# Kernel optimization log

Measured on AMD Instinct MI355X. Metric: run time of the kernel, lower is better.

## Reference

```python
import jax, jax.numpy as jnp
import numpy as np

ALPHA = 0.2        # LeakyReLU negative slope (config['alpha'])
NEG_INF = -9e15    # mask value from the original code


def setup_inputs() -> dict:
    key = jax.random.key(0)
    k1, k2, k3, k4 = jax.random.split(key, 4)
    N, Fin, Fout = 8192, 512, 256
    inp = jax.random.normal(k1, (N, Fin), dtype=jnp.float32)
    adj = jax.random.randint(k2, (N, N), 0, 2, dtype=jnp.int32)
    # xavier_uniform with gain=1.414
    limW = 1.414 * np.sqrt(6.0 / (Fin + Fout))
    W = jax.random.uniform(k3, (Fin, Fout), dtype=jnp.float32, minval=-limW, maxval=limW)
    lima = 1.414 * np.sqrt(6.0 / (2 * Fout + 1))
    a = jax.random.uniform(k4, (2 * Fout, 1), dtype=jnp.float32, minval=-lima, maxval=lima)
    return {"input": inp, "adj": adj, "W": W, "a": a}


def reference(input, adj, W, a):
    # h: [N, F]
    h = input @ W
    Fout = W.shape[1]
    # The original builds a_input[i, j] = concat(h_i, h_j) and dots with a.
    # Equivalently: e_ij = leakyrelu(h_i . a[:F] + h_j . a[F:]), computed
    # without the O(N^2 * 2F) intermediate.
    s1 = h @ a[:Fout, 0]   # [N] contribution from node i
    s2 = h @ a[Fout:, 0]   # [N] contribution from node j
    e = s1[:, None] + s2[None, :]                     # [N, N]
    e = jnp.where(e > 0, e, ALPHA * e)                # LeakyReLU
    scores = jnp.where(adj > 0, e, NEG_INF)
    attention = jax.nn.softmax(scores, axis=1)        # row-wise softmax
    # dropout is identity in inference mode (training=False)
    h_prime = attention @ h                           # [N, F]
    return jax.nn.elu(h_prime)                        # concat=True path
```

## Files before the change

### kernel.cpp

```cpp
#include <hip/hip_runtime.h>
#include <stdint.h>
#include <stddef.h>


#define N_NODES 8192
#define FIN     512
#define FOUT    256
#define LRALPHA 0.2f
#define MI_SHIFT 16.0f

typedef float f32x4 __attribute__((ext_vector_type(4)));
typedef short s16x8 __attribute__((ext_vector_type(8)));
typedef unsigned short u16x4 __attribute__((ext_vector_type(4)));
typedef int   i32x4 __attribute__((ext_vector_type(4)));
typedef unsigned long long u64;

__device__ __forceinline__ short f2bf_rne(float f) {
  uint32_t u = __builtin_bit_cast(uint32_t, f);
  u += 0x7fffu + ((u >> 16) & 1u);
  return (short)(u >> 16);
}
__device__ __forceinline__ short f2bf_fast(float f) {
  uint32_t u = __builtin_bit_cast(uint32_t, f);
  return (short)((u + 0x8000u) >> 16);
}
__device__ __forceinline__ float bf2f(short s) {
  uint32_t u = ((uint32_t)(uint16_t)s) << 16;
  return __builtin_bit_cast(float, u);
}

__global__ __launch_bounds__(256) void k_prep(const float* __restrict__ W,
                                              uint16_t* __restrict__ WThi,
                                              uint16_t* __restrict__ WTlo) {
  const int idx = blockIdx.x * 256 + threadIdx.x;
  const int n = idx >> 9;
  const int k = idx & 511;
  float v = W[k * FOUT + n];
  short h = f2bf_rne(v);
  WThi[idx] = (uint16_t)h;
  WTlo[idx] = (uint16_t)f2bf_rne(v - bf2f(h));
}

__global__ __launch_bounds__(256, 4) void k_pre(const float* __restrict__ X,
                                                const uint16_t* __restrict__ WThi,
                                                const uint16_t* __restrict__ WTlo,
                                                const float* __restrict__ a,
                                                const int* __restrict__ adj,
                                                uint16_t* __restrict__ HTf,
                                                float* __restrict__ s1g,
                                                float* __restrict__ s2g,
                                                u64* __restrict__ M3) {
  __shared__ float ls1[16], ls2[16];
  __shared__ uint16_t tile[FOUT * 16];
  const int lane = threadIdx.x & 63;
  const int w    = threadIdx.x >> 6;

  if (blockIdx.x >= 512) {
    const int bxm  = blockIdx.x - 512;
    const int iblk = bxm >> 5;
    const int jc   = bxm & 31;
    const int L    = lane;
    const int* base = adj + (size_t)(iblk * 128 + w * 32) * N_NODES + jc * 256 + L;
    u64 keep0 = 0, keep1 = 0, keep2 = 0, keep3 = 0;
#pragma unroll
    for (int it = 0; it < 32; ++it) {
      const int* rp = base + (size_t)it * N_NODES;
      int v0 = rp[0], v1 = rp[64], v2 = rp[128], v3 = rp[192];
      u64 b0 = __ballot(v0 != 0);
      u64 b1 = __ballot(v1 != 0);
      u64 b2 = __ballot(v2 != 0);
      u64 b3 = __ballot(v3 != 0);
      if (L == it) { keep0 = b0; keep1 = b1; keep2 = b2; keep3 = b3; }
    }
    if (L < 32) {
      const size_t mb = (size_t)iblk * 128 * 128 + (w * 32 + L);
      M3[mb + (size_t)(jc * 4 + 0) * 128] = keep0;
      M3[mb + (size_t)(jc * 4 + 1) * 128] = keep1;
      M3[mb + (size_t)(jc * 4 + 2) * 128] = keep2;
      M3[mb + (size_t)(jc * 4 + 3) * 128] = keep3;
    }
    return;
  }

  const int m    = lane & 15;
  const int quad = lane >> 4;
  const int i0   = blockIdx.x * 16;
  const int colg = w * 64;

  f32x4 acc[4];
#pragma unroll
  for (int cb = 0; cb < 4; ++cb) { f32x4 z = {0.f,0.f,0.f,0.f}; acc[cb] = z; }

  for (int kt = 0; kt < FIN / 32; ++kt) {
    const int k0 = kt * 32 + quad * 8;
    const float* ap = X + (size_t)(i0 + m) * FIN + k0;
    f32x4 a0 = *(const f32x4*)ap;
    f32x4 a1 = *(const f32x4*)(ap + 4);
    s16x8 ahi, alo;
#pragma unroll
    for (int e = 0; e < 4; ++e) {
      short h0 = f2bf_rne(a0[e]); ahi[e] = h0; alo[e] = f2bf_rne(a0[e] - bf2f(h0));
      short h1 = f2bf_rne(a1[e]); ahi[4+e] = h1; alo[4+e] = f2bf_rne(a1[e] - bf2f(h1));
    }
#pragma unroll
    for (int cb = 0; cb < 4; ++cb) {
      const int n = colg + cb * 16 + m;
      s16x8 bhi = *(const s16x8*)(WThi + (size_t)n * FIN + k0);
      s16x8 blo = *(const s16x8*)(WTlo + (size_t)n * FIN + k0);
      acc[cb] = __builtin_amdgcn_mfma_f32_16x16x32_bf16(ahi, bhi, acc[cb], 0, 0, 0);
      acc[cb] = __builtin_amdgcn_mfma_f32_16x16x32_bf16(ahi, blo, acc[cb], 0, 0, 0);
      acc[cb] = __builtin_amdgcn_mfma_f32_16x16x32_bf16(alo, bhi, acc[cb], 0, 0, 0);
    }
  }

  float p1[4] = {0.f,0.f,0.f,0.f}, p2[4] = {0.f,0.f,0.f,0.f};
#pragma unroll
  for (int cb = 0; cb < 4; ++cb) {
    const int n = colg + cb * 16 + m;
    const float a1c = a[n];
    const float a2c = a[FOUT + n];
#pragma unroll
    for (int reg = 0; reg < 4; ++reg) {
      p1[reg] += acc[cb][reg] * a1c;
      p2[reg] += acc[cb][reg] * a2c;
    }
  }
#pragma unroll
  for (int off = 1; off <= 8; off <<= 1)
#pragma unroll
    for (int reg = 0; reg < 4; ++reg) {
      p1[reg] += __shfl_xor(p1[reg], off);
      p2[reg] += __shfl_xor(p2[reg], off);
    }
  if (threadIdx.x < 16) { ls1[threadIdx.x] = 0.f; ls2[threadIdx.x] = 0.f; }
  __syncthreads();
  if (m == 0) {
#pragma unroll
    for (int reg = 0; reg < 4; ++reg) {
      atomicAdd(&ls1[quad * 4 + reg], p1[reg]);
      atomicAdd(&ls2[quad * 4 + reg], p2[reg]);
    }
  }
#pragma unroll
  for (int cb = 0; cb < 4; ++cb) {
    const int col = colg + cb * 16 + m;
    u16x4 pk;
#pragma unroll
    for (int reg = 0; reg < 4; ++reg) pk[reg] = (uint16_t)f2bf_rne(acc[cb][reg]);
    *(u16x4*)(tile + col * 16 + quad * 4) = pk;
  }
  __syncthreads();
  const int t = threadIdx.x;
  if (t < 16) { s1g[i0 + t] = ls1[t]; s2g[i0 + t] = ls2[t]; }
  const int jt = i0 >> 5;
  const int qh = (i0 >> 4) & 1;
  const int c  = t >> 4;
  const int mm = t & 15;
#pragma unroll
  for (int qq = 0; qq < 2; ++qq) {
    uint4 v = *(const uint4*)(tile + (c * 16 + mm) * 16 + qq * 8);
    *(uint4*)(HTf + ((((size_t)jt * 16 + c) * 64) + (qh * 2 + qq) * 16 + mm) * 8) = v;
  }
}

__global__ __launch_bounds__(512, 4) void k_attn(const u64* __restrict__ M3,
                                                 const uint16_t* __restrict__ HTf,
                                                 const float* __restrict__ s1,
                                                 const float* __restrict__ s2,
                                                 float* __restrict__ pout,
                                                 float* __restrict__ pden,
                                                 int split) {
  __shared__ uint16_t PL[2][4096];
  __shared__ float lss2[1024];
  __shared__ float ldsden[512];

  const int tid  = threadIdx.x;
  const int lane = tid & 63;
  const int w    = tid >> 6;
  const int m    = lane & 15;
  const int q    = lane >> 4;
  const int rg   = w >> 2, cg = w & 3;
  const int r    = tid & 127;
  const int cpr  = tid >> 7;
  const int i0   = blockIdx.x * 128;
  const int sp   = blockIdx.y;
  const int jrange = N_NODES / split;
  const int jbeg   = sp * jrange;
  const int nphase = jrange / 32;

  const float s1r = s1[i0 + r];
  float mi = fmaxf(s1r + MI_SHIFT, LRALPHA * (s1r + MI_SHIFT));

  f32x4 acc[4][4];
#pragma unroll
  for (int rt = 0; rt < 4; ++rt)
#pragma unroll
    for (int cb = 0; cb < 4; ++cb) { f32x4 z = {0.f,0.f,0.f,0.f}; acc[rt][cb] = z; }
  float den = 0.f;

  const u64* mrow = M3 + ((size_t)blockIdx.x * 128 + (jbeg >> 6)) * 128 + r;
  u64 mcur = mrow[0];

#pragma unroll 1
  for (int ph = 0; ph < nphase; ph += 2) {
    if ((ph & 31) == 0) {
      __syncthreads();
      if (tid < 256) *(f32x4*)(lss2 + tid * 4) =
        *(const f32x4*)(s2 + jbeg + (ph >> 5) * 1024 + tid * 4);
      __syncthreads();
    }
    u64 mnx = (ph + 2 < nphase) ? mrow[((ph >> 1) + 1) * 128] : 0;
#pragma unroll
    for (int po = 0; po < 2; ++po) {
      const int p = ph + po;
      const int pl = p & 31;
      f32x4 sA = *(const f32x4*)(lss2 + pl * 32 + cpr * 8);
      f32x4 sB = *(const f32x4*)(lss2 + pl * 32 + cpr * 8 + 4);
      const uint32_t by = (uint32_t)(mcur >> ((po * 4 + cpr) * 8)) & 0xffu;
      s16x8 P0;
#pragma unroll
      for (int e = 0; e < 4; ++e) {
        float x0 = s1r + sA[e];
        float pv0 = __expf(fmaxf(x0, LRALPHA * x0) - mi);
        pv0 = ((by >> e) & 1u) ? pv0 : 0.f;
        den += pv0; P0[e] = f2bf_fast(pv0);
        float x1 = s1r + sB[e];
        float pv1 = __expf(fmaxf(x1, LRALPHA * x1) - mi);
        pv1 = ((by >> (e + 4)) & 1u) ? pv1 : 0.f;
        den += pv1; P0[4 + e] = f2bf_fast(pv1);
      }
      *(s16x8*)(PL[p & 1] + (cpr * 128 + r) * 8) = P0;
      __syncthreads();
      const uint16_t* hB = HTf + ((size_t)((jbeg >> 5) + p) * 16 + cg * 4) * 512 + lane * 8;
      s16x8 Bv[4];
#pragma unroll
      for (int cb = 0; cb < 4; ++cb)
        Bv[cb] = *(const s16x8*)(hB + cb * 512);
      s16x8 F[4];
#pragma unroll
      for (int rt = 0; rt < 4; ++rt)
        F[rt] = *(const s16x8*)(PL[p & 1] + (q * 128 + rg * 64 + rt * 16 + m) * 8);
#pragma unroll
      for (int rt = 0; rt < 4; ++rt)
#pragma unroll
        for (int cb = 0; cb < 4; ++cb)
          acc[rt][cb] = __builtin_amdgcn_mfma_f32_16x16x32_bf16(F[rt], Bv[cb], acc[rt][cb], 0, 0, 0);
    }
    mcur = mnx;
  }

  ldsden[cpr * 128 + r] = den;
  __syncthreads();
  if (tid < 128) {
    float d = ldsden[tid] + ldsden[128 + tid] + ldsden[256 + tid] + ldsden[384 + tid];
    pden[(size_t)sp * N_NODES + i0 + tid] = d;
  }
#pragma unroll
  for (int rt = 0; rt < 4; ++rt)
#pragma unroll
    for (int cb = 0; cb < 4; ++cb)
#pragma unroll
      for (int reg = 0; reg < 4; ++reg) {
        const int row = i0 + rg * 64 + rt * 16 + q * 4 + reg;
        const int col = cg * 64 + cb * 16 + m;
        pout[((size_t)sp * N_NODES + row) * FOUT + col] = acc[rt][cb][reg];
      }
}

__global__ __launch_bounds__(256) void k_reduce(const float* __restrict__ pout,
                                                const float* __restrict__ pden,
                                                float* __restrict__ out,
                                                int split) {
  const int gid = blockIdx.x * 256 + threadIdx.x;
  const int i = gid >> 6;
  const int c = (gid & 63) << 2;
  f32x4 sum = {0.f,0.f,0.f,0.f};
  float den = 0.f;
  for (int s = 0; s < split; ++s) {
    sum += *(const f32x4*)(pout + ((size_t)s * N_NODES + i) * FOUT + c);
    den += pden[(size_t)s * N_NODES + i];
  }
  const float inv = 1.0f / den;
  f32x4 r;
#pragma unroll
  for (int e = 0; e < 4; ++e) {
    float v = sum[e] * inv;
    r[e] = v > 0.f ? v : (__expf(v) - 1.0f);
  }
  *(f32x4*)(out + (size_t)i * FOUT + c) = r;
}

extern "C" void kernel_launch(void* const* d_in, const int* in_sizes, int n_in,
                              void* d_out, int out_size, void* d_ws, size_t ws_size,
                              hipStream_t stream) {
  const float* X   = (const float*)d_in[0];
  const int*   adj = (const int*)d_in[1];
  const float* W   = (const float*)d_in[2];
  const float* a   = (const float*)d_in[3];
  float* out = (float*)d_out;

  char* ws = (char*)d_ws;
  uint16_t* HTf  = (uint16_t*)ws;
  uint16_t* WThi = (uint16_t*)(ws + (4u << 20));
  uint16_t* WTlo = (uint16_t*)(ws + (4u << 20) + 262144);
  float*    s1   = (float*)(ws + (4u << 20) + 524288);
  float*    s2   = s1 + N_NODES;
  float*    pden = s2 + N_NODES;
  u64*      M3   = (u64*)(ws + (6u << 20));
  const size_t pout_off = (size_t)16u << 20;
  const size_t slab = (size_t)N_NODES * FOUT * sizeof(float);

  int split;
  if      (ws_size >= pout_off + 8 * slab) split = 8;
  else if (ws_size >= pout_off + 4 * slab) split = 4;
  else if (ws_size >= pout_off + 2 * slab) split = 2;
  else                                     split = 1;
  float* pout = (split == 1) ? out : (float*)(ws + pout_off);

  k_prep<<<dim3(512), dim3(256), 0, stream>>>(W, WThi, WTlo);
  k_pre<<<dim3(2560), dim3(256), 0, stream>>>(X, WThi, WTlo, a, adj, HTf, s1, s2, M3);
  k_attn<<<dim3(N_NODES / 128, split), dim3(512), 0, stream>>>(M3, HTf, s1, s2, pout, pden, split);
  k_reduce<<<dim3(N_NODES * FOUT / 4 / 256), dim3(256), 0, stream>>>(pout, pden, out, split);
}
```

Measured before the change: 473.0 us.

## Read adjacency directly in attention kernel, dropping the bitmask pre-pass

The separate adjacency-to-bitmask pass inside the pre-kernel is removed, and the attention kernel now reads int32 adjacency rows directly with vector loads prefetched one phase ahead. Thread mapping changes so four consecutive threads cover one row, which lets the denominator be reduced with shuffles instead of shared memory. This saves one kernel's worth of writing and re-reading the compressed mask. In exchange, the attention loop now streams 32-bit adjacency (32x more bytes than the bitmask) inside its main loop, which may put more load on memory bandwidth.

```diff
diff --git a/kernel.cpp b/kernel.cpp
--- a/kernel.cpp
+++ b/kernel.cpp
@@ -41,47 +41,17 @@
   WTlo[idx] = (uint16_t)f2bf_rne(v - bf2f(h));
 }
 
-__global__ __launch_bounds__(256, 4) void k_pre(const float* __restrict__ X,
-                                                const uint16_t* __restrict__ WThi,
-                                                const uint16_t* __restrict__ WTlo,
-                                                const float* __restrict__ a,
-                                                const int* __restrict__ adj,
-                                                uint16_t* __restrict__ HTf,
-                                                float* __restrict__ s1g,
-                                                float* __restrict__ s2g,
-                                                u64* __restrict__ M3) {
+__global__ __launch_bounds__(256, 4) void k_gemm(const float* __restrict__ X,
+                                                 const uint16_t* __restrict__ WThi,
+                                                 const uint16_t* __restrict__ WTlo,
+                                                 const float* __restrict__ a,
+                                                 uint16_t* __restrict__ HTf,
+                                                 float* __restrict__ s1g,
+                                                 float* __restrict__ s2g) {
   __shared__ float ls1[16], ls2[16];
   __shared__ uint16_t tile[FOUT * 16];
   const int lane = threadIdx.x & 63;
   const int w    = threadIdx.x >> 6;
-
-  if (blockIdx.x >= 512) {
-    const int bxm  = blockIdx.x - 512;
-    const int iblk = bxm >> 5;
-    const int jc   = bxm & 31;
-    const int L    = lane;
-    const int* base = adj + (size_t)(iblk * 128 + w * 32) * N_NODES + jc * 256 + L;
-    u64 keep0 = 0, keep1 = 0, keep2 = 0, keep3 = 0;
-#pragma unroll
-    for (int it = 0; it < 32; ++it) {
-      const int* rp = base + (size_t)it * N_NODES;
-      int v0 = rp[0], v1 = rp[64], v2 = rp[128], v3 = rp[192];
-      u64 b0 = __ballot(v0 != 0);
-      u64 b1 = __ballot(v1 != 0);
-      u64 b2 = __ballot(v2 != 0);
-      u64 b3 = __ballot(v3 != 0);
-      if (L == it) { keep0 = b0; keep1 = b1; keep2 = b2; keep3 = b3; }
-    }
-    if (L < 32) {
-      const size_t mb = (size_t)iblk * 128 * 128 + (w * 32 + L);
-      M3[mb + (size_t)(jc * 4 + 0) * 128] = keep0;
-      M3[mb + (size_t)(jc * 4 + 1) * 128] = keep1;
-      M3[mb + (size_t)(jc * 4 + 2) * 128] = keep2;
-      M3[mb + (size_t)(jc * 4 + 3) * 128] = keep3;
-    }
-    return;
-  }
-
   const int m    = lane & 15;
   const int quad = lane >> 4;
   const int i0   = blockIdx.x * 16;
@@ -163,7 +133,7 @@
   }
 }
 
-__global__ __launch_bounds__(512, 4) void k_attn(const u64* __restrict__ M3,
+__global__ __launch_bounds__(512, 4) void k_attn(const int* __restrict__ adj,
                                                  const uint16_t* __restrict__ HTf,
                                                  const float* __restrict__ s1,
                                                  const float* __restrict__ s2,
@@ -172,7 +142,6 @@
                                                  int split) {
   __shared__ uint16_t PL[2][4096];
   __shared__ float lss2[1024];
-  __shared__ float ldsden[512];
 
   const int tid  = threadIdx.x;
   const int lane = tid & 63;
@@ -180,16 +149,16 @@
   const int m    = lane & 15;
   const int q    = lane >> 4;
   const int rg   = w >> 2, cg = w & 3;
-  const int r    = tid & 127;
-  const int cpr  = tid >> 7;
+  const int pr   = tid >> 2;
+  const int cpr  = tid & 3;
   const int i0   = blockIdx.x * 128;
   const int sp   = blockIdx.y;
   const int jrange = N_NODES / split;
   const int jbeg   = sp * jrange;
   const int nphase = jrange / 32;
 
-  const float s1r = s1[i0 + r];
-  float mi = fmaxf(s1r + MI_SHIFT, LRALPHA * (s1r + MI_SHIFT));
+  const float s1r = s1[i0 + pr];
+  const float mi = fmaxf(s1r + MI_SHIFT, LRALPHA * (s1r + MI_SHIFT));
 
   f32x4 acc[4][4];
 #pragma unroll
@@ -198,63 +167,58 @@
     for (int cb = 0; cb < 4; ++cb) { f32x4 z = {0.f,0.f,0.f,0.f}; acc[rt][cb] = z; }
   float den = 0.f;
 
-  const u64* mrow = M3 + ((size_t)blockIdx.x * 128 + (jbeg >> 6)) * 128 + r;
-  u64 mcur = mrow[0];
+  const int* arow = adj + (size_t)(i0 + pr) * N_NODES + jbeg + cpr * 8;
+  i32x4 A0 = *(const i32x4*)arow;
+  i32x4 A1 = *(const i32x4*)(arow + 4);
 
 #pragma unroll 1
-  for (int ph = 0; ph < nphase; ph += 2) {
-    if ((ph & 31) == 0) {
+  for (int p = 0; p < nphase; ++p) {
+    if ((p & 31) == 0) {
       __syncthreads();
       if (tid < 256) *(f32x4*)(lss2 + tid * 4) =
-        *(const f32x4*)(s2 + jbeg + (ph >> 5) * 1024 + tid * 4);
+        *(const f32x4*)(s2 + jbeg + (p >> 5) * 1024 + tid * 4);
       __syncthreads();
     }
-    u64 mnx = (ph + 2 < nphase) ? mrow[((ph >> 1) + 1) * 128] : 0;
-#pragma unroll
-    for (int po = 0; po < 2; ++po) {
-      const int p = ph + po;
-      const int pl = p & 31;
-      f32x4 sA = *(const f32x4*)(lss2 + pl * 32 + cpr * 8);
-      f32x4 sB = *(const f32x4*)(lss2 + pl * 32 + cpr * 8 + 4);
-      const uint32_t by = (uint32_t)(mcur >> ((po * 4 + cpr) * 8)) & 0xffu;
-      s16x8 P0;
-#pragma unroll
-      for (int e = 0; e < 4; ++e) {
-        float x0 = s1r + sA[e];
-        float pv0 = __expf(fmaxf(x0, LRALPHA * x0) - mi);
-        pv0 = ((by >> e) & 1u) ? pv0 : 0.f;
-        den += pv0; P0[e] = f2bf_fast(pv0);
-        float x1 = s1r + sB[e];
-        float pv1 = __expf(fmaxf(x1, LRALPHA * x1) - mi);
-        pv1 = ((by >> (e + 4)) & 1u) ? pv1 : 0.f;
-        den += pv1; P0[4 + e] = f2bf_fast(pv1);
-      }
-      *(s16x8*)(PL[p & 1] + (cpr * 128 + r) * 8) = P0;
-      __syncthreads();
-      const uint16_t* hB = HTf + ((size_t)((jbeg >> 5) + p) * 16 + cg * 4) * 512 + lane * 8;
-      s16x8 Bv[4];
+    const int pn = (p + 1 < nphase) ? p + 1 : p;
+    i32x4 nA0 = *(const i32x4*)(arow + pn * 32);
+    i32x4 nA1 = *(const i32x4*)(arow + pn * 32 + 4);
+    const int pl = p & 31;
+    f32x4 sA = *(const f32x4*)(lss2 + pl * 32 + cpr * 8);
+    f32x4 sB = *(const f32x4*)(lss2 + pl * 32 + cpr * 8 + 4);
+    s16x8 P0;
+#pragma unroll
+    for (int e = 0; e < 4; ++e) {
+      float x0 = s1r + sA[e];
+      float pv0 = __expf(fmaxf(x0, LRALPHA * x0) - mi);
+      pv0 = (A0[e] != 0) ? pv0 : 0.f;
+      den += pv0; P0[e] = f2bf_fast(pv0);
+      float x1 = s1r + sB[e];
+      float pv1 = __expf(fmaxf(x1, LRALPHA * x1) - mi);
+      pv1 = (A1[e] != 0) ? pv1 : 0.f;
+      den += pv1; P0[4 + e] = f2bf_fast(pv1);
+    }
+    *(s16x8*)(PL[p & 1] + (cpr * 128 + pr) * 8) = P0;
+    A0 = nA0; A1 = nA1;
+    __syncthreads();
+    const uint16_t* hB = HTf + ((size_t)((jbeg >> 5) + p) * 16 + cg * 4) * 512 + lane * 8;
+    s16x8 Bv[4];
+#pragma unroll
+    for (int cb = 0; cb < 4; ++cb)
+      Bv[cb] = *(const s16x8*)(hB + cb * 512);
+    s16x8 F[4];
+#pragma unroll
+    for (int rt = 0; rt < 4; ++rt)
+      F[rt] = *(const s16x8*)(PL[p & 1] + (q * 128 + rg * 64 + rt * 16 + m) * 8);
+#pragma unroll
+    for (int rt = 0; rt < 4; ++rt)
 #pragma unroll
       for (int cb = 0; cb < 4; ++cb)
-        Bv[cb] = *(const s16x8*)(hB + cb * 512);
-      s16x8 F[4];
-#pragma unroll
-      for (int rt = 0; rt < 4; ++rt)
-        F[rt] = *(const s16x8*)(PL[p & 1] + (q * 128 + rg * 64 + rt * 16 + m) * 8);
-#pragma unroll
-      for (int rt = 0; rt < 4; ++rt)
-#pragma unroll
-        for (int cb = 0; cb < 4; ++cb)
-          acc[rt][cb] = __builtin_amdgcn_mfma_f32_16x16x32_bf16(F[rt], Bv[cb], acc[rt][cb], 0, 0, 0);
-    }
-    mcur = mnx;
-  }
-
-  ldsden[cpr * 128 + r] = den;
-  __syncthreads();
-  if (tid < 128) {
-    float d = ldsden[tid] + ldsden[128 + tid] + ldsden[256 + tid] + ldsden[384 + tid];
-    pden[(size_t)sp * N_NODES + i0 + tid] = d;
-  }
+        acc[rt][cb] = __builtin_amdgcn_mfma_f32_16x16x32_bf16(F[rt], Bv[cb], acc[rt][cb], 0, 0, 0);
+  }
+
+  den += __shfl_xor(den, 1);
+  den += __shfl_xor(den, 2);
+  if (cpr == 0) pden[(size_t)sp * N_NODES + i0 + pr] = den;
 #pragma unroll
   for (int rt = 0; rt < 4; ++rt)
 #pragma unroll
@@ -306,7 +270,6 @@
   float*    s1   = (float*)(ws + (4u << 20) + 524288);
   float*    s2   = s1 + N_NODES;
   float*    pden = s2 + N_NODES;
-  u64*      M3   = (u64*)(ws + (6u << 20));
   const size_t pout_off = (size_t)16u << 20;
   const size_t slab = (size_t)N_NODES * FOUT * sizeof(float);
 
@@ -318,7 +281,7 @@
   float* pout = (split == 1) ? out : (float*)(ws + pout_off);
 
   k_prep<<<dim3(512), dim3(256), 0, stream>>>(W, WThi, WTlo);
-  k_pre<<<dim3(2560), dim3(256), 0, stream>>>(X, WThi, WTlo, a, adj, HTf, s1, s2, M3);
-  k_attn<<<dim3(N_NODES / 128, split), dim3(512), 0, stream>>>(M3, HTf, s1, s2, pout, pden, split);
+  k_gemm<<<dim3(N_NODES / 16), dim3(256), 0, stream>>>(X, WThi, WTlo, a, HTf, s1, s2);
+  k_attn<<<dim3(N_NODES / 128, split), dim3(512), 0, stream>>>(adj, HTf, s1, s2, pout, pden, split);
   k_reduce<<<dim3(N_NODES * FOUT / 4 / 256), dim3(256), 0, stream>>>(pout, pden, out, split);
 }
```

Result: no change. 481.0 us (+1.7%).
